# Kernel tuning notes

Measured on AMD Instinct MI355X. Metric: run time of the kernel, lower is better.

The kernel has to match this reference:

```python
import jax, jax.numpy as jnp
import numpy as np

D_MODEL = 128
N_HEADS = 4
HEAD_DIM = D_MODEL // N_HEADS


def setup_inputs() -> dict:
    key = jax.random.key(0)
    ks = jax.random.split(key, 16)
    s = 0.05
    B, N, T = 1, 1024, 1024
    return {
        "node_states": jax.random.normal(ks[0], (B, N, D_MODEL), jnp.float32),
        "task_features": jax.random.normal(ks[1], (T, D_MODEL), jnp.float32),
        "in_proj_w": jax.random.normal(ks[2], (3 * D_MODEL, D_MODEL), jnp.float32) * s,
        "in_proj_b": jnp.zeros((3 * D_MODEL,), jnp.float32),
        "out_w": jax.random.normal(ks[3], (D_MODEL, D_MODEL), jnp.float32) * s,
        "out_b": jnp.zeros((D_MODEL,), jnp.float32),
        "W1": jax.random.normal(ks[4], (256, 256), jnp.float32) * s,
        "b1": jnp.zeros((256,), jnp.float32),
        "W2": jax.random.normal(ks[5], (128, 256), jnp.float32) * s,
        "b2": jnp.zeros((128,), jnp.float32),
        "W3": jax.random.normal(ks[6], (1, 128), jnp.float32) * s,
        "b3": jnp.zeros((1,), jnp.float32),
        "Wc1": jax.random.normal(ks[7], (256, D_MODEL), jnp.float32) * s,
        "bc1": jnp.zeros((256,), jnp.float32),
        "Wc2": jax.random.normal(ks[8], (32, 256), jnp.float32) * s,
        "bc2": jnp.zeros((32,), jnp.float32),
    }


def _mha(x, in_proj_w, in_proj_b, out_w, out_b):
    # x: [B, N, D]; torch nn.MultiheadAttention self-attention, batch_first.
    B, N, D = x.shape
    q = x @ in_proj_w[:D].T + in_proj_b[:D]
    k = x @ in_proj_w[D:2 * D].T + in_proj_b[D:2 * D]
    v = x @ in_proj_w[2 * D:].T + in_proj_b[2 * D:]
    def split(t):  # [B,N,D] -> [B,H,N,dh]
        return t.reshape(B, N, N_HEADS, HEAD_DIM).transpose(0, 2, 1, 3)
    qh, kh, vh = split(q), split(k), split(v)
    scores = jnp.einsum("bhqd,bhkd->bhqk", qh, kh) / jnp.sqrt(jnp.float32(HEAD_DIM))
    attn = jax.nn.softmax(scores, axis=-1)  # [B,H,N,N]
    ctx = jnp.einsum("bhqk,bhkd->bhqd", attn, vh)
    ctx = ctx.transpose(0, 2, 1, 3).reshape(B, N, D)
    out = ctx @ out_w.T + out_b
    attn_avg = attn.mean(axis=1)  # torch averages heads by default -> [B,N,N]
    return out, attn_avg


def reference(node_states, task_features, in_proj_w, in_proj_b, out_w, out_b,
              W1, b1, W2, b2, W3, b3, Wc1, bc1, Wc2, bc2):
    attended, attn_w = _mha(node_states, in_proj_w, in_proj_b, out_w, out_b)
    nodes = attended[0]  # original loop only uses batch 0: [N, D]
    # Linear on concat([task, node]) == split-weight sum; vectorize pairwise.
    t1 = task_features @ W1[:, :D_MODEL].T          # [T, 256]
    n1 = nodes @ W1[:, D_MODEL:].T                  # [N, 256]
    h1 = jax.nn.relu(t1[:, None, :] + n1[None, :, :] + b1)      # [T, N, 256]
    h2 = jax.nn.relu(jnp.einsum("tnc,kc->tnk", h1, W2) + b2)   # [T, N, 128]
    matching_scores = jax.nn.sigmoid(jnp.einsum("tnk,ok->tn", h2, W3) + b3[0])
    global_state = attended.mean(axis=1)            # [B, D]
    coordination_logits = jax.nn.relu(global_state @ Wc1.T + bc1) @ Wc2.T + bc2
    return matching_scores, coordination_logits, attn_w
```

## Files before the change

kernel.cpp:

```cpp
#include <hip/hip_runtime.h>
#include <hip/hip_fp16.h>
#include <stdint.h>


typedef __attribute__((ext_vector_type(4))) float floatx4;
typedef __attribute__((ext_vector_type(8))) _Float16 half8;

#define OFF_QKV  0x000000u
#define OFF_Q16  0x180000u
#define OFF_K16  0x1C0000u
#define OFF_V16  0x200000u
#define OFF_T1H  0x280000u
#define OFF_N1H  0x300000u
#define OFF_W2F  0x380000u
#define OFF_GS   0x398000u

__device__ __forceinline__ unsigned pkadd(unsigned a, unsigned b) {
    unsigned r; asm("v_pk_add_f16 %0, %1, %2" : "=v"(r) : "v"(a), "v"(b)); return r;
}
__device__ __forceinline__ unsigned pkmax(unsigned a, unsigned b) {
    unsigned r; asm("v_pk_max_f16 %0, %1, %2" : "=v"(r) : "v"(a), "v"(b)); return r;
}
__device__ __forceinline__ unsigned pk2h(float a, float b) {
    return (unsigned)__half_as_ushort(__float2half(a)) |
           ((unsigned)__half_as_ushort(__float2half(b)) << 16);
}
__device__ __forceinline__ float h2f(unsigned short u) {
    return __half2float(__ushort_as_half(u));
}
__device__ __forceinline__ unsigned short f2h(float v) {
    return __half_as_ushort(__float2half(v));
}
__device__ __forceinline__ int plds(int row, int kb) {
    return row * 2048 + (((kb & ~15) ^ ((row & 7) << 4))) + (kb & 15);
}

template<bool BIAS, bool F16OUT, bool SIDE>
__device__ __forceinline__ void gemm_dev(
    const float* __restrict__ A, int lda,
    const float* __restrict__ B, int ldb,
    const float* __restrict__ bias,
    void* __restrict__ Cv, int ldc, int K, float scale,
    int m0, int n0, float (*As)[64], float (*Bs)[64],
    unsigned short* __restrict__ q16o,
    unsigned short* __restrict__ k16o,
    unsigned short* __restrict__ v16o)
{
    const int tid = threadIdx.x;
    const int tx = tid & 15, ty = tid >> 4;
    const int lr = tid >> 2;
    const int lk = (tid & 3) * 4;
    float c[4][4] = {};

    for (int k0 = 0; k0 < K; k0 += 16) {
        float4 a  = *(const float4*)&A[(long)(m0 + lr) * lda + k0 + lk];
        float4 bb = *(const float4*)&B[(long)(n0 + lr) * ldb + k0 + lk];
        __syncthreads();
        As[lk + 0][lr] = a.x;  As[lk + 1][lr] = a.y;  As[lk + 2][lr] = a.z;  As[lk + 3][lr] = a.w;
        Bs[lk + 0][lr] = bb.x; Bs[lk + 1][lr] = bb.y; Bs[lk + 2][lr] = bb.z; Bs[lk + 3][lr] = bb.w;
        __syncthreads();
#pragma unroll
        for (int k = 0; k < 16; k++) {
            float4 av = *(const float4*)&As[k][ty * 4];
            float4 bv = *(const float4*)&Bs[k][tx * 4];
            c[0][0] += av.x * bv.x; c[0][1] += av.x * bv.y; c[0][2] += av.x * bv.z; c[0][3] += av.x * bv.w;
            c[1][0] += av.y * bv.x; c[1][1] += av.y * bv.y; c[1][2] += av.y * bv.z; c[1][3] += av.y * bv.w;
            c[2][0] += av.z * bv.x; c[2][1] += av.z * bv.y; c[2][2] += av.z * bv.z; c[2][3] += av.z * bv.w;
            c[3][0] += av.w * bv.x; c[3][1] += av.w * bv.y; c[3][2] += av.w * bv.z; c[3][3] += av.w * bv.w;
        }
    }

    float bsv[4] = {0.f, 0.f, 0.f, 0.f};
    if (BIAS) {
        float4 t = *(const float4*)&bias[n0 + tx * 4];
        bsv[0] = t.x; bsv[1] = t.y; bsv[2] = t.z; bsv[3] = t.w;
    }
    const int gcol = n0 + tx * 4;
#pragma unroll
    for (int i = 0; i < 4; i++) {
        float v0 = c[i][0] * scale + bsv[0];
        float v1 = c[i][1] * scale + bsv[1];
        float v2 = c[i][2] * scale + bsv[2];
        float v3 = c[i][3] * scale + bsv[3];
        long m = m0 + ty * 4 + i;
        if (F16OUT) {
            unsigned short* Cp = (unsigned short*)Cv;
            ushort4 o;
            o.x = f2h(v0); o.y = f2h(v1); o.z = f2h(v2); o.w = f2h(v3);
            *(ushort4*)&Cp[m * ldc + n0 + tx * 4] = o;
        } else {
            float* Cp = (float*)Cv;
            *(float4*)&Cp[m * ldc + n0 + tx * 4] = make_float4(v0, v1, v2, v3);
        }
        if (SIDE) {
            ushort4 o;
            o.x = f2h(v0); o.y = f2h(v1); o.z = f2h(v2); o.w = f2h(v3);
            if (gcol < 128) {
                *(ushort4*)&q16o[m * 128 + gcol] = o;
            } else if (gcol < 256) {
                *(ushort4*)&k16o[m * 128 + (gcol - 128)] = o;
            } else {
                v16o[(size_t)(gcol - 256 + 0) * 1024 + m] = o.x;
                v16o[(size_t)(gcol - 256 + 1) * 1024 + m] = o.y;
                v16o[(size_t)(gcol - 256 + 2) * 1024 + m] = o.z;
                v16o[(size_t)(gcol - 256 + 3) * 1024 + m] = o.w;
            }
        }
    }
}

__launch_bounds__(256)
__global__ void proj_fused(const float* __restrict__ node, const float* __restrict__ ipw,
                           const float* __restrict__ ipb,
                           const float* __restrict__ task, const float* __restrict__ W1,
                           const float* __restrict__ b1, const float* __restrict__ W2,
                           float* __restrict__ qkv, unsigned short* __restrict__ t1h,
                           unsigned short* __restrict__ w2f, float* __restrict__ gs,
                           unsigned short* __restrict__ q16,
                           unsigned short* __restrict__ k16,
                           unsigned short* __restrict__ v16t)
{
    __shared__ float As[16][64], Bs[16][64];
    const int bid = blockIdx.x;
    if (bid < 96) {
        gemm_dev<true, false, true>(node, 128, ipw, 128, ipb, qkv, 384, 128, 1.0f,
                                    (bid & 15) * 64, (bid >> 4) * 64, As, Bs,
                                    q16, k16, v16t);
    } else if (bid < 160) {
        const int b = bid - 96;
        gemm_dev<true, true, false>(task, 128, W1, 256, b1, t1h, 256, 128, 1.0f,
                                    (b & 15) * 64, (b >> 4) * 64, As, Bs,
                                    nullptr, nullptr, nullptr);
    } else if (bid < 176) {
        const int gtid = (bid - 160) * 256 + threadIdx.x;
        const int lane = gtid & 63, frag = gtid >> 6;
        const int cc = frag >> 3, ot = frag & 7;
        const float* src = &W2[(ot * 16 + (lane & 15)) * 256 + cc * 32 + (lane >> 4) * 8];
        uint4 o;
        o.x = pk2h(src[0], src[1]);
        o.y = pk2h(src[2], src[3]);
        o.z = pk2h(src[4], src[5]);
        o.w = pk2h(src[6], src[7]);
        ((uint4*)w2f)[gtid] = o;
    } else {
        if (threadIdx.x < 128) gs[threadIdx.x] = 0.f;
    }
}

__launch_bounds__(512)
__global__ void attn_one(const unsigned short* __restrict__ q16,
                         const unsigned short* __restrict__ k16,
                         const unsigned short* __restrict__ v16t,
                         const float* __restrict__ outw, const float* __restrict__ outb,
                         const float* __restrict__ W1,
                         unsigned short* __restrict__ n1h, float* __restrict__ gs,
                         float* __restrict__ attn_out)
{
    extern __shared__ char smem[];
    float* ctx2 = (float*)(smem + 131072);
    float* il   = (float*)(smem + 147456);
    float* attr = (float*)smem;

    const int tid = threadIdx.x;
    const int q0 = blockIdx.x * 16;
    const int lane = tid & 63, wv = tid >> 6;
    const int col = lane & 15, quad = lane >> 4;
    const int h = wv & 3, khalf = wv >> 2;
    const int prow = h * 16 + col;

    {
        union { uint4 u; half8 h8; } bq;
        bq.u = *(const uint4*)&q16[(size_t)(q0 + col) * 128 + h * 32 + quad * 8];
        for (int kt = khalf * 32; kt < khalf * 32 + 32; kt++) {
            union { uint4 u; half8 h8; } ak;
            ak.u = *(const uint4*)&k16[(size_t)(kt * 16 + col) * 128 + h * 32 + quad * 8];
            floatx4 c = {0.f, 0.f, 0.f, 0.f};
            c = __builtin_amdgcn_mfma_f32_16x16x32_f16(ak.h8, bq.h8, c, 0, 0, 0);
            ushort4 o;
            o.x = f2h(c[0] * 0.17677669529663687f);
            o.y = f2h(c[1] * 0.17677669529663687f);
            o.z = f2h(c[2] * 0.17677669529663687f);
            o.w = f2h(c[3] * 0.17677669529663687f);
            *(ushort4*)(smem + plds(prow, kt * 32 + quad * 8)) = o;
        }
    }
    __syncthreads();

    {
        const int row = tid >> 3, oct = tid & 7;
        char* rb = smem + row * 2048;
        const int swz = (row & 7) << 4;
        float mx = -1e30f;
#pragma unroll
        for (int i = 0; i < 16; i++) {
            uint4 v = *(uint4*)(rb + ((oct * 256 + i * 16) ^ swz));
            const unsigned short* pv = (const unsigned short*)&v;
#pragma unroll
            for (int j = 0; j < 8; j++) mx = fmaxf(mx, h2f(pv[j]));
        }
        mx = fmaxf(mx, __shfl_xor(mx, 1));
        mx = fmaxf(mx, __shfl_xor(mx, 2));
        mx = fmaxf(mx, __shfl_xor(mx, 4));
        float s = 0.f;
#pragma unroll
        for (int i = 0; i < 16; i++) {
            char* ap = rb + ((oct * 256 + i * 16) ^ swz);
            uint4 v = *(uint4*)ap;
            const unsigned short* pv = (const unsigned short*)&v;
            ushort4 w0, w1;
            float p0 = __expf(h2f(pv[0]) - mx), p1 = __expf(h2f(pv[1]) - mx);
            float p2 = __expf(h2f(pv[2]) - mx), p3 = __expf(h2f(pv[3]) - mx);
            float p4 = __expf(h2f(pv[4]) - mx), p5 = __expf(h2f(pv[5]) - mx);
            float p6 = __expf(h2f(pv[6]) - mx), p7 = __expf(h2f(pv[7]) - mx);
            s += p0 + p1 + p2 + p3 + p4 + p5 + p6 + p7;
            w0.x = f2h(p0); w0.y = f2h(p1); w0.z = f2h(p2); w0.w = f2h(p3);
            w1.x = f2h(p4); w1.y = f2h(p5); w1.z = f2h(p6); w1.w = f2h(p7);
            *(ushort4*)ap = w0;
            *(ushort4*)(ap + 8) = w1;
        }
        s += __shfl_xor(s, 1);
        s += __shfl_xor(s, 2);
        s += __shfl_xor(s, 4);
        if ((tid & 7) == 0) il[row] = 1.0f / s;
    }
    __syncthreads();

    {
        floatx4 acc[2] = {};
        for (int ks = khalf * 16; ks < khalf * 16 + 16; ks++) {
            union { uint4 u; half8 h8; } pf;
            pf.u = *(uint4*)(smem + plds(prow, ks * 64 + quad * 16));
#pragma unroll
            for (int dt = 0; dt < 2; dt++) {
                union { uint4 u; half8 h8; } vf;
                vf.u = *(const uint4*)&v16t[(size_t)(h * 32 + dt * 16 + col) * 1024 + ks * 32 + quad * 8];
                acc[dt] = __builtin_amdgcn_mfma_f32_16x16x32_f16(vf.h8, pf.h8, acc[dt], 0, 0, 0);
            }
        }
        const float sil = il[prow];
#pragma unroll
        for (int dt = 0; dt < 2; dt++) {
            *(float4*)&ctx2[(khalf * 16 + col) * 128 + h * 32 + dt * 16 + quad * 4] =
                make_float4(acc[dt][0] * sil, acc[dt][1] * sil, acc[dt][2] * sil, acc[dt][3] * sil);
        }
    }
    {
        const int q = tid >> 5, kc = tid & 31;
        const float s0 = il[q] * 0.25f, s1 = il[16 + q] * 0.25f;
        const float s2 = il[32 + q] * 0.25f, s3 = il[48 + q] * 0.25f;
#pragma unroll
        for (int b = 0; b < 4; b++) {
            const int kb = kc * 64 + b * 16;
            uint4 v0 = *(uint4*)(smem + plds(q, kb));
            uint4 v1 = *(uint4*)(smem + plds(16 + q, kb));
            uint4 v2 = *(uint4*)(smem + plds(32 + q, kb));
            uint4 v3 = *(uint4*)(smem + plds(48 + q, kb));
            const unsigned short* p0 = (const unsigned short*)&v0;
            const unsigned short* p1 = (const unsigned short*)&v1;
            const unsigned short* p2 = (const unsigned short*)&v2;
            const unsigned short* p3 = (const unsigned short*)&v3;
            float o[8];
#pragma unroll
            for (int j = 0; j < 8; j++)
                o[j] = h2f(p0[j]) * s0 + h2f(p1[j]) * s1 + h2f(p2[j]) * s2 + h2f(p3[j]) * s3;
            float* dst = &attn_out[(size_t)(q0 + q) * 1024 + kc * 32 + b * 8];
            *(float4*)dst = make_float4(o[0], o[1], o[2], o[3]);
            *(float4*)(dst + 4) = make_float4(o[4], o[5], o[6], o[7]);
        }
    }
    __syncthreads();

    {
        const int j = tid & 127, qh = tid >> 7;
        float a0 = outb[j], a1 = a0, a2 = a0, a3 = a0;
        const float* wr = &outw[j * 128];
        for (int d = 0; d < 128; d += 4) {
            float4 w = *(const float4*)&wr[d];
#pragma unroll
            for (int qq = 0; qq < 4; qq++) {
                const int q = qh * 4 + qq;
                float4 c0 = *(const float4*)&ctx2[q * 128 + d];
                float4 c1 = *(const float4*)&ctx2[(16 + q) * 128 + d];
                float dot = w.x * (c0.x + c1.x) + w.y * (c0.y + c1.y)
                          + w.z * (c0.z + c1.z) + w.w * (c0.w + c1.w);
                if (qq == 0) a0 += dot; else if (qq == 1) a1 += dot;
                else if (qq == 2) a2 += dot; else a3 += dot;
            }
        }
        attr[(qh * 4 + 0) * 128 + j] = a0;
        attr[(qh * 4 + 1) * 128 + j] = a1;
        attr[(qh * 4 + 2) * 128 + j] = a2;
        attr[(qh * 4 + 3) * 128 + j] = a3;
    }
    __syncthreads();

    if (tid < 128) {
        float s = 0.f;
#pragma unroll
        for (int q = 0; q < 16; q++) s += attr[q * 128 + tid];
        atomicAdd(&gs[tid], s);
    }
    {
        const int c = tid & 255, qh = tid >> 8;
        const float* wr = &W1[c * 256 + 128];
        float n[8] = {};
        for (int d = 0; d < 128; d += 4) {
            float4 w = *(const float4*)&wr[d];
#pragma unroll
            for (int qq = 0; qq < 8; qq++) {
                float4 a = *(const float4*)&attr[(qh * 8 + qq) * 128 + d];
                n[qq] += w.x * a.x + w.y * a.y + w.z * a.z + w.w * a.w;
            }
        }
#pragma unroll
        for (int qq = 0; qq < 8; qq++)
            n1h[(size_t)(q0 + qh * 8 + qq) * 256 + c] = f2h(n[qq]);
    }
}

__launch_bounds__(256, 2)
__global__ void score_kernel(const unsigned short* __restrict__ t1h,
                             const unsigned short* __restrict__ n1h,
                             const unsigned short* __restrict__ w2f,
                             const float* __restrict__ b2, const float* __restrict__ W3,
                             const float* __restrict__ b3, float* __restrict__ out,
                             const float* __restrict__ gs,
                             const float* __restrict__ Wc1, const float* __restrict__ bc1,
                             const float* __restrict__ Wc2, const float* __restrict__ bc2,
                             float* __restrict__ outc)
{
    __shared__ unsigned short w2s[32768];
    __shared__ float b2s[128], w3s[128];
    const int tid = threadIdx.x;

    if (blockIdx.y == 32) {
        if (blockIdx.x != 0) return;
        float* g  = (float*)w2s;
        float* hh = g + 128;
        if (tid < 128) g[tid] = gs[tid] * (1.0f / 1024.0f);
        __syncthreads();
        {
            float a = bc1[tid];
            const float* wr = &Wc1[tid * 128];
            for (int d = 0; d < 128; d += 4) {
                float4 w = *(const float4*)&wr[d];
                a += w.x * g[d] + w.y * g[d + 1] + w.z * g[d + 2] + w.w * g[d + 3];
            }
            hh[tid] = fmaxf(a, 0.f);
        }
        __syncthreads();
        if (tid < 32) {
            float a = bc2[tid];
            const float* wr = &Wc2[tid * 256];
            for (int c = 0; c < 256; c += 4) {
                float4 w = *(const float4*)&wr[c];
                a += w.x * hh[c] + w.y * hh[c + 1] + w.z * hh[c + 2] + w.w * hh[c + 3];
            }
            outc[tid] = a;
        }
        return;
    }

    const int lane = tid & 63;
    const int wv = tid >> 6;
    const int col = lane & 15;
    const int quad = lane >> 4;
    const int nb = blockIdx.x * 64 + wv * 16;
    const int tb = blockIdx.y * 32;

    {
        const uint4* src = (const uint4*)w2f;
        uint4* dst = (uint4*)w2s;
#pragma unroll
        for (int i = 0; i < 16; i++) dst[tid + i * 256] = src[tid + i * 256];
        if (tid < 128) { b2s[tid] = b2[tid]; w3s[tid] = W3[tid]; }
    }

    const unsigned short* nbase = n1h + (size_t)(nb + col) * 256 + quad * 8;
    const unsigned short* tbase = t1h + (size_t)tb * 256 + quad * 8;
    const float b3s = b3[0];
    __syncthreads();

    uint4 np_c = *(const uint4*)(nbase);
    uint4 tp_c[4];
#pragma unroll
    for (int tt = 0; tt < 4; tt++)
        tp_c[tt] = *(const uint4*)(tbase + (size_t)tt * 256);

    for (int tg = 0; tg < 8; tg++) {
        floatx4 acc[4][8];
#pragma unroll
        for (int ot = 0; ot < 8; ot++) {
            float4 bq = *(const float4*)&b2s[ot * 16 + quad * 4];
            floatx4 bi = {bq.x, bq.y, bq.z, bq.w};
#pragma unroll
            for (int tt = 0; tt < 4; tt++) acc[tt][ot] = bi;
        }

#pragma unroll
        for (int cc = 0; cc < 8; cc++) {
            const int ncc = (cc + 1) & 7;
            const int ntg = (cc == 7) ? ((tg + 1) & 7) : tg;
            uint4 np_n = *(const uint4*)(nbase + ncc * 32);
            uint4 tp_n[4];
#pragma unroll
            for (int tt = 0; tt < 4; tt++)
                tp_n[tt] = *(const uint4*)(tbase + (size_t)(ntg * 4 + tt) * 256 + ncc * 32);

            const unsigned* npu = (const unsigned*)&np_c;
            union { unsigned u[4]; half8 h; } af[4];
#pragma unroll
            for (int tt = 0; tt < 4; tt++) {
                const unsigned* tpu = (const unsigned*)&tp_c[tt];
#pragma unroll
                for (int p = 0; p < 4; p++)
                    af[tt].u[p] = pkmax(pkadd(tpu[p], npu[p]), 0u);
            }
            __builtin_amdgcn_s_setprio(1);
#pragma unroll
            for (int ot = 0; ot < 8; ot++) {
                union { uint4 u; half8 h; } bf;
                bf.u = *(const uint4*)&w2s[((cc * 8 + ot) * 64 + lane) * 8];
#pragma unroll
                for (int tt = 0; tt < 4; tt++)
                    acc[tt][ot] = __builtin_amdgcn_mfma_f32_16x16x32_f16(bf.h, af[tt].h, acc[tt][ot], 0, 0, 0);
            }
            __builtin_amdgcn_s_setprio(0);

            np_c = np_n;
#pragma unroll
            for (int tt = 0; tt < 4; tt++) tp_c[tt] = tp_n[tt];
        }

        float part[4] = {0.f, 0.f, 0.f, 0.f};
#pragma unroll
        for (int ot = 0; ot < 8; ot++) {
            float4 wq = *(const float4*)&w3s[ot * 16 + quad * 4];
#pragma unroll
            for (int tt = 0; tt < 4; tt++) {
                floatx4 a = acc[tt][ot];
                part[tt] += fmaxf(a[0], 0.f) * wq.x + fmaxf(a[1], 0.f) * wq.y
                          + fmaxf(a[2], 0.f) * wq.z + fmaxf(a[3], 0.f) * wq.w;
            }
        }
        float outv = 0.f;
#pragma unroll
        for (int tt = 0; tt < 4; tt++) {
            float p = part[tt];
            p += __shfl_xor(p, 16);
            p += __shfl_xor(p, 32);
            if (quad == tt) outv = p;
        }
        out[(size_t)(tb + tg * 4 + quad) * 1024 + nb + col] =
            1.0f / (1.0f + __expf(-(outv + b3s)));
    }
}

extern "C" void kernel_launch(void* const* d_in, const int* in_sizes, int n_in,
                              void* d_out, int out_size, void* d_ws, size_t ws_size,
                              hipStream_t stream)
{
    const float* node = (const float*)d_in[0];
    const float* task = (const float*)d_in[1];
    const float* ipw  = (const float*)d_in[2];
    const float* ipb  = (const float*)d_in[3];
    const float* outw = (const float*)d_in[4];
    const float* outb = (const float*)d_in[5];
    const float* W1   = (const float*)d_in[6];
    const float* b1   = (const float*)d_in[7];
    const float* W2   = (const float*)d_in[8];
    const float* b2   = (const float*)d_in[9];
    const float* W3   = (const float*)d_in[10];
    const float* b3   = (const float*)d_in[11];
    const float* Wc1  = (const float*)d_in[12];
    const float* bc1  = (const float*)d_in[13];
    const float* Wc2  = (const float*)d_in[14];
    const float* bc2  = (const float*)d_in[15];

    char* ws = (char*)d_ws;
    float* qkv = (float*)(ws + OFF_QKV);
    unsigned short* q16 = (unsigned short*)(ws + OFF_Q16);
    unsigned short* k16 = (unsigned short*)(ws + OFF_K16);
    unsigned short* v16t = (unsigned short*)(ws + OFF_V16);
    unsigned short* t1h = (unsigned short*)(ws + OFF_T1H);
    unsigned short* n1h = (unsigned short*)(ws + OFF_N1H);
    unsigned short* w2f = (unsigned short*)(ws + OFF_W2F);
    float* gs = (float*)(ws + OFF_GS);

    float* out_match = (float*)d_out;
    float* out_coord = out_match + 1048576;
    float* out_attn  = out_coord + 32;

    static bool attr_set = false;
    if (!attr_set) {
        hipFuncSetAttribute((const void*)attn_one,
                            hipFuncAttributeMaxDynamicSharedMemorySize, 147712);
        attr_set = true;
    }

    proj_fused<<<dim3(177, 1, 1), 256, 0, stream>>>(
        node, ipw, ipb, task, W1, b1, W2, qkv, t1h, w2f, gs, q16, k16, v16t);
    attn_one<<<dim3(64, 1, 1), 512, 147712, stream>>>(
        q16, k16, v16t, outw, outb, W1, n1h, gs, out_attn);
    score_kernel<<<dim3(16, 33, 1), 256, 0, stream>>>(
        t1h, n1h, w2f, b2, W3, b3, out_match,
        gs, Wc1, bc1, Wc2, bc2, out_coord);
}
```

Measured before the change: 203.8 us.

## Switch score kernel to 32x32x16 MFMA tiles with reshaped W2 fragments

Replaces the 16x16x32 MFMA tiling in the pairwise scoring kernel with 32x32x16 MFMA. Each wave now covers 32 nodes by 2 tasks per step, and the W2 fp16 fragment layout is rewritten to match. The bias is now added in the epilogue instead of initialising the accumulators, the register prefetch of the next chunk's inputs is dropped, and the grid changes from 16x33 to 8x65. The aim is fewer MFMA issues and less A-operand construction per FLOP. The trade-off is losing the explicit load prefetch and the s_setprio hints, which may expose global-load latency.

```diff
diff --git a/kernel.cpp b/kernel.cpp
--- a/kernel.cpp
+++ b/kernel.cpp
@@ -4,6 +4,7 @@
 
 
 typedef __attribute__((ext_vector_type(4))) float floatx4;
+typedef __attribute__((ext_vector_type(16))) float floatx16;
 typedef __attribute__((ext_vector_type(8))) _Float16 half8;
 
 #define OFF_QKV  0x000000u
@@ -134,8 +135,8 @@
     } else if (bid < 176) {
         const int gtid = (bid - 160) * 256 + threadIdx.x;
         const int lane = gtid & 63, frag = gtid >> 6;
-        const int cc = frag >> 3, ot = frag & 7;
-        const float* src = &W2[(ot * 16 + (lane & 15)) * 256 + cc * 32 + (lane >> 4) * 8];
+        const int ks = frag >> 2, ot = frag & 3;
+        const float* src = &W2[(ot * 32 + (lane & 31)) * 256 + ks * 16 + (lane >> 5) * 8];
         uint4 o;
         o.x = pk2h(src[0], src[1]);
         o.y = pk2h(src[2], src[3]);
@@ -333,7 +334,7 @@
     __shared__ float b2s[128], w3s[128];
     const int tid = threadIdx.x;
 
-    if (blockIdx.y == 32) {
+    if (blockIdx.y == 64) {
         if (blockIdx.x != 0) return;
         float* g  = (float*)w2s;
         float* hh = g + 128;
@@ -363,10 +364,10 @@
 
     const int lane = tid & 63;
     const int wv = tid >> 6;
-    const int col = lane & 15;
-    const int quad = lane >> 4;
-    const int nb = blockIdx.x * 64 + wv * 16;
-    const int tb = blockIdx.y * 32;
+    const int nc = lane & 31;
+    const int ko = lane >> 5;
+    const int nb = blockIdx.x * 128 + wv * 32;
+    const int tb = blockIdx.y * 16;
 
     {
         const uint4* src = (const uint4*)w2f;
@@ -376,83 +377,65 @@
         if (tid < 128) { b2s[tid] = b2[tid]; w3s[tid] = W3[tid]; }
     }
 
-    const unsigned short* nbase = n1h + (size_t)(nb + col) * 256 + quad * 8;
-    const unsigned short* tbase = t1h + (size_t)tb * 256 + quad * 8;
+    const unsigned short* nbase = n1h + (size_t)(nb + nc) * 256 + ko * 8;
+    const unsigned short* tbase = t1h + (size_t)tb * 256 + ko * 8;
     const float b3s = b3[0];
     __syncthreads();
 
-    uint4 np_c = *(const uint4*)(nbase);
-    uint4 tp_c[4];
-#pragma unroll
-    for (int tt = 0; tt < 4; tt++)
-        tp_c[tt] = *(const uint4*)(tbase + (size_t)tt * 256);
-
     for (int tg = 0; tg < 8; tg++) {
-        floatx4 acc[4][8];
-#pragma unroll
-        for (int ot = 0; ot < 8; ot++) {
-            float4 bq = *(const float4*)&b2s[ot * 16 + quad * 4];
-            floatx4 bi = {bq.x, bq.y, bq.z, bq.w};
-#pragma unroll
-            for (int tt = 0; tt < 4; tt++) acc[tt][ot] = bi;
-        }
-
-#pragma unroll
-        for (int cc = 0; cc < 8; cc++) {
-            const int ncc = (cc + 1) & 7;
-            const int ntg = (cc == 7) ? ((tg + 1) & 7) : tg;
-            uint4 np_n = *(const uint4*)(nbase + ncc * 32);
-            uint4 tp_n[4];
-#pragma unroll
-            for (int tt = 0; tt < 4; tt++)
-                tp_n[tt] = *(const uint4*)(tbase + (size_t)(ntg * 4 + tt) * 256 + ncc * 32);
-
-            const unsigned* npu = (const unsigned*)&np_c;
-            union { unsigned u[4]; half8 h; } af[4];
-#pragma unroll
-            for (int tt = 0; tt < 4; tt++) {
-                const unsigned* tpu = (const unsigned*)&tp_c[tt];
-#pragma unroll
-                for (int p = 0; p < 4; p++)
-                    af[tt].u[p] = pkmax(pkadd(tpu[p], npu[p]), 0u);
-            }
-            __builtin_amdgcn_s_setprio(1);
-#pragma unroll
-            for (int ot = 0; ot < 8; ot++) {
+        floatx16 acc[2][4] = {};
+
+#pragma unroll
+        for (int ks = 0; ks < 16; ks++) {
+            uint4 np  = *(const uint4*)(nbase + ks * 16);
+            uint4 tp0 = *(const uint4*)(tbase + (size_t)(tg * 2 + 0) * 256 + ks * 16);
+            uint4 tp1 = *(const uint4*)(tbase + (size_t)(tg * 2 + 1) * 256 + ks * 16);
+
+            const unsigned* npu = (const unsigned*)&np;
+            const unsigned* t0u = (const unsigned*)&tp0;
+            const unsigned* t1u = (const unsigned*)&tp1;
+            union { unsigned u[4]; half8 h; } af0, af1;
+#pragma unroll
+            for (int p = 0; p < 4; p++) {
+                af0.u[p] = pkmax(pkadd(t0u[p], npu[p]), 0u);
+                af1.u[p] = pkmax(pkadd(t1u[p], npu[p]), 0u);
+            }
+#pragma unroll
+            for (int ot = 0; ot < 4; ot++) {
                 union { uint4 u; half8 h; } bf;
-                bf.u = *(const uint4*)&w2s[((cc * 8 + ot) * 64 + lane) * 8];
-#pragma unroll
-                for (int tt = 0; tt < 4; tt++)
-                    acc[tt][ot] = __builtin_amdgcn_mfma_f32_16x16x32_f16(bf.h, af[tt].h, acc[tt][ot], 0, 0, 0);
-            }
-            __builtin_amdgcn_s_setprio(0);
-
-            np_c = np_n;
-#pragma unroll
-            for (int tt = 0; tt < 4; tt++) tp_c[tt] = tp_n[tt];
-        }
-
-        float part[4] = {0.f, 0.f, 0.f, 0.f};
-#pragma unroll
-        for (int ot = 0; ot < 8; ot++) {
-            float4 wq = *(const float4*)&w3s[ot * 16 + quad * 4];
-#pragma unroll
-            for (int tt = 0; tt < 4; tt++) {
-                floatx4 a = acc[tt][ot];
-                part[tt] += fmaxf(a[0], 0.f) * wq.x + fmaxf(a[1], 0.f) * wq.y
-                          + fmaxf(a[2], 0.f) * wq.z + fmaxf(a[3], 0.f) * wq.w;
-            }
-        }
-        float outv = 0.f;
-#pragma unroll
-        for (int tt = 0; tt < 4; tt++) {
-            float p = part[tt];
-            p += __shfl_xor(p, 16);
-            p += __shfl_xor(p, 32);
-            if (quad == tt) outv = p;
-        }
-        out[(size_t)(tb + tg * 4 + quad) * 1024 + nb + col] =
-            1.0f / (1.0f + __expf(-(outv + b3s)));
+                bf.u = *(const uint4*)&w2s[((ks * 4 + ot) * 64 + lane) * 8];
+                acc[0][ot] = __builtin_amdgcn_mfma_f32_32x32x16_f16(bf.h, af0.h, acc[0][ot], 0, 0, 0);
+                acc[1][ot] = __builtin_amdgcn_mfma_f32_32x32x16_f16(bf.h, af1.h, acc[1][ot], 0, 0, 0);
+            }
+        }
+
+        float part0 = 0.f, part1 = 0.f;
+#pragma unroll
+        for (int ot = 0; ot < 4; ot++) {
+            floatx16 a0 = acc[0][ot];
+            floatx16 a1 = acc[1][ot];
+#pragma unroll
+            for (int g = 0; g < 4; g++) {
+                float4 bq = *(const float4*)&b2s[ot * 32 + g * 8 + ko * 4];
+                float4 wq = *(const float4*)&w3s[ot * 32 + g * 8 + ko * 4];
+                part0 += fmaxf(a0[g * 4 + 0] + bq.x, 0.f) * wq.x
+                       + fmaxf(a0[g * 4 + 1] + bq.y, 0.f) * wq.y
+                       + fmaxf(a0[g * 4 + 2] + bq.z, 0.f) * wq.z
+                       + fmaxf(a0[g * 4 + 3] + bq.w, 0.f) * wq.w;
+                part1 += fmaxf(a1[g * 4 + 0] + bq.x, 0.f) * wq.x
+                       + fmaxf(a1[g * 4 + 1] + bq.y, 0.f) * wq.y
+                       + fmaxf(a1[g * 4 + 2] + bq.z, 0.f) * wq.z
+                       + fmaxf(a1[g * 4 + 3] + bq.w, 0.f) * wq.w;
+            }
+        }
+        part0 += __shfl_xor(part0, 32);
+        part1 += __shfl_xor(part1, 32);
+        if (lane < 32) {
+            out[(size_t)(tb + tg * 2 + 0) * 1024 + nb + nc] =
+                1.0f / (1.0f + __expf(-(part0 + b3s)));
+            out[(size_t)(tb + tg * 2 + 1) * 1024 + nb + nc] =
+                1.0f / (1.0f + __expf(-(part1 + b3s)));
+        }
     }
 }
 
@@ -502,7 +485,7 @@
         node, ipw, ipb, task, W1, b1, W2, qkv, t1h, w2f, gs, q16, k16, v16t);
     attn_one<<<dim3(64, 1, 1), 512, 147712, stream>>>(
         q16, k16, v16t, outw, outb, W1, n1h, gs, out_attn);
-    score_kernel<<<dim3(16, 33, 1), 256, 0, stream>>>(
+    score_kernel<<<dim3(8, 65, 1), 256, 0, stream>>>(
         t1h, n1h, w2f, b2, W3, b3, out_match,
         gs, Wc1, bc1, Wc2, bc2, out_coord);
 }
```

Result: no change. 205.6 us (+0.9%).
